# Kernel optimization log

Hardware: AMD Instinct MI355X
Metric: run time of the kernel (lower is better)

The kernel has to match this reference:

```python
import jax, jax.numpy as jnp
import numpy as np
from jax import lax

B, H, W, C = 2, 256, 256, 180
WS, SH, NH = 8, 4, 6
HD = C // NH          # 30
N = WS * WS           # 64
NW = (H // WS) * (W // WS)
HID = 4 * C
SCALE = HD ** -0.5
EPS = 1e-5


def _rel_pos_index(ws):
    coords = np.stack(np.meshgrid(np.arange(ws), np.arange(ws), indexing='ij'))  # [2,ws,ws]
    cf = coords.reshape(2, -1)
    rel = (cf[:, :, None] - cf[:, None, :]).transpose(1, 2, 0)  # [N,N,2]
    rel[:, :, 0] += ws - 1
    rel[:, :, 1] += ws - 1
    rel[:, :, 0] *= 2 * ws - 1
    return rel.sum(-1)  # [N,N]


def _attn_mask(h, w, ws, sh):
    img = np.zeros((h, w))
    sl = (slice(0, -ws), slice(-ws, -sh), slice(-sh, None))
    cnt = 0
    for hs in sl:
        for wsl in sl:
            img[hs, wsl] = cnt
            cnt += 1
    mw = img.reshape(h // ws, ws, w // ws, ws).transpose(0, 2, 1, 3).reshape(-1, ws * ws)  # [nW,N]
    d = mw[:, None, :] - mw[:, :, None]  # [nW,N,N]
    return np.where(d != 0, -100.0, 0.0).astype(np.float32)


REL_IDX = jnp.asarray(_rel_pos_index(WS))          # [N,N] int
MASK = jnp.asarray(_attn_mask(H, W, WS, SH))       # [nW,N,N] float


def _ln(x, g, b):
    m = jnp.mean(x, -1, keepdims=True)
    v = jnp.mean((x - m) ** 2, -1, keepdims=True)
    return (x - m) * lax.rsqrt(v + EPS) * g + b


def _win_part(x):  # (B,H,W,C) -> (B*nW,N,C)
    x = x.reshape(B, H // WS, WS, W // WS, WS, C).transpose(0, 1, 3, 2, 4, 5)
    return x.reshape(-1, N, C)


def _win_rev(w):  # (B*nW,N,C) -> (B,H,W,C)
    x = w.reshape(B, H // WS, W // WS, WS, WS, C).transpose(0, 1, 3, 2, 4, 5)
    return x.reshape(B, H, W, C)


def setup_inputs() -> dict:
    key = jax.random.key(0)
    ks = jax.random.split(key, 8)
    s = 0.02
    return {
        'x': jax.random.normal(ks[0], (B, H * W, C), jnp.float32),
        'norm1_g': jnp.ones((C,), jnp.float32),
        'norm1_b': jnp.zeros((C,), jnp.float32),
        'qkv_w': jax.random.normal(ks[1], (C, 3 * C), jnp.float32) * s,
        'qkv_b': jnp.zeros((3 * C,), jnp.float32),
        'rel_pos_table': jax.random.normal(ks[2], ((2 * WS - 1) ** 2, NH), jnp.float32) * s,
        'proj_w': jax.random.normal(ks[3], (C, C), jnp.float32) * s,
        'proj_b': jnp.zeros((C,), jnp.float32),
        'norm2_g': jnp.ones((C,), jnp.float32),
        'norm2_b': jnp.zeros((C,), jnp.float32),
        'fc1_w': jax.random.normal(ks[4], (C, HID), jnp.float32) * s,
        'fc1_b': jnp.zeros((HID,), jnp.float32),
        'dw_w': jax.random.normal(ks[5], (HID, 1, 3, 3), jnp.float32) * s,
        'dw_b': jnp.zeros((HID,), jnp.float32),
        'fc2_w': jax.random.normal(ks[6], (HID, C), jnp.float32) * s,
        'fc2_b': jnp.zeros((C,), jnp.float32),
    }


def reference(x, norm1_g, norm1_b, qkv_w, qkv_b, rel_pos_table, proj_w, proj_b,
              norm2_g, norm2_b, fc1_w, fc1_b, dw_w, dw_b, fc2_w, fc2_b):
    shortcut = x
    h = _ln(x, norm1_g, norm1_b).reshape(B, H, W, C)
    h = jnp.roll(h, (-SH, -SH), axis=(1, 2))           # cyclic shift
    xw = _win_part(h)                                   # [B*nW, N, C]

    qkv = (xw @ qkv_w + qkv_b).reshape(-1, N, 3, NH, HD).transpose(2, 0, 3, 1, 4)
    q, k, v = qkv[0] * SCALE, qkv[1], qkv[2]            # [B_,NH,N,HD]
    attn = jnp.einsum('bhnd,bhmd->bhnm', q, k)          # [B_,NH,N,N]

    bias = rel_pos_table[REL_IDX.reshape(-1)].reshape(N, N, NH).transpose(2, 0, 1)
    attn = attn + bias[None]
    attn = attn.reshape(B, NW, NH, N, N) + MASK[None, :, None]
    attn = jax.nn.softmax(attn.reshape(-1, NH, N, N), axis=-1)

    out = jnp.einsum('bhnm,bhmd->bhnd', attn, v).transpose(0, 2, 1, 3).reshape(-1, N, C)
    out = out @ proj_w + proj_b
    out = jnp.roll(_win_rev(out), (SH, SH), axis=(1, 2)).reshape(B, H * W, C)
    x = shortcut + out

    # MLP with depthwise-conv interleave
    m = _ln(x, norm2_g, norm2_b)
    m = jax.nn.gelu(m @ fc1_w + fc1_b, approximate=False)   # [B,L,HID]
    mc = m.transpose(0, 2, 1).reshape(B, HID, H, W)
    mc = lax.conv_general_dilated(mc, dw_w, (1, 1), 'SAME',
                                  feature_group_count=HID,
                                  dimension_numbers=('NCHW', 'OIHW', 'NCHW'))
    mc = mc + dw_b[None, :, None, None]
    m = jax.nn.gelu(mc.reshape(B, HID, H * W).transpose(0, 2, 1), approximate=False)
    m = m @ fc2_w + fc2_b
    return x + m
```

## Files before the change

### kernel.cpp

```cpp
#include <hip/hip_runtime.h>
#include <hip/hip_bf16.h>


using short8 = __attribute__((ext_vector_type(8))) short;
using f32x4  = __attribute__((ext_vector_type(4))) float;

constexpr int   ROWS   = 131072;
constexpr float SCALE_ = 0.18257418583505536f;

constexpr size_t OFF_WQ    = 0;
constexpr size_t OFF_WP    = OFF_WQ   + 576*192*2;
constexpr size_t OFF_WF1   = OFF_WP   + 192*192*2;
constexpr size_t OFF_WF2T  = OFF_WF1  + 768*192*2;
constexpr size_t OFF_BQ    = OFF_WF2T + 192*768*2;
constexpr size_t OFF_BP    = OFF_BQ   + 576*4;
constexpr size_t OFF_BF1   = OFF_BP   + 192*4;
constexpr size_t OFF_BF2   = OFF_BF1  + 768*4;
constexpr size_t OFF_BIASF = OFF_BF2  + 192*4;
constexpr size_t OFF_WDWT  = OFF_BIASF + 6*4096*4;
constexpr size_t OFF_BDW   = OFF_WDWT + 9*768*4;
constexpr size_t OFF_R1    = 1048576;
constexpr size_t SZ_R      = (size_t)ROWS * 192 * 2;
constexpr size_t OFF_R2    = OFF_R1 + SZ_R;
constexpr size_t OFF_R3    = OFF_R2 + SZ_R;
constexpr size_t WS_NEEDED = OFF_R3 + SZ_R;
static_assert(OFF_BDW + 768*4 <= OFF_R1, "weights overlap R1");
static_assert((size_t)66*256*768*2 <= SZ_R, "m1 band overflows R2");

__device__ __forceinline__ unsigned short f2bf(float f) {
    __hip_bfloat16 h = __float2bfloat16(f);
    return *reinterpret_cast<unsigned short*>(&h);
}
__device__ __forceinline__ float bf2f(unsigned short u) {
    union { unsigned int i; float f; } x; x.i = ((unsigned int)u) << 16; return x.f;
}
__device__ __forceinline__ float gelu_f(float x) {
    return 0.5f * x * (1.0f + erff(x * 0.70710678118654752f));
}

__global__ __launch_bounds__(256) void prep_kernel(
    const float* __restrict__ qkv_w, const float* __restrict__ qkv_b,
    const float* __restrict__ proj_w, const float* __restrict__ proj_b,
    const float* __restrict__ fc1_w, const float* __restrict__ fc1_b,
    const float* __restrict__ fc2_w, const float* __restrict__ fc2_b,
    const float* __restrict__ rpt,
    const float* __restrict__ dw_w, const float* __restrict__ dw_b,
    unsigned short* __restrict__ wq, unsigned short* __restrict__ wp,
    unsigned short* __restrict__ wf1, unsigned short* __restrict__ wf2t,
    float* __restrict__ bq, float* __restrict__ bp,
    float* __restrict__ bf1, float* __restrict__ bf2,
    float* __restrict__ biasf,
    float* __restrict__ wdwT, float* __restrict__ bdw)
{
    int idx = blockIdx.x * 256 + threadIdx.x;
    constexpr int E1 = 576*192;
    constexpr int E2 = E1 + 192*192;
    constexpr int E3 = E2 + 768*192;
    constexpr int E4 = E3 + 192*768;
    constexpr int E5 = E4 + 576;
    constexpr int E6 = E5 + 192;
    constexpr int E7 = E6 + 768;
    constexpr int E8 = E7 + 192;
    constexpr int E9 = E8 + 6*4096;
    constexpr int E10 = E9 + 9*768;
    constexpr int E11 = E10 + 768;
    if (idx < E1) {
        int n = idx / 192, kx = idx % 192;
        float v = 0.f;
        if (n < 540 && kx < 180) { v = qkv_w[kx*540 + n]; if (n < 180) v *= SCALE_; }
        wq[idx] = f2bf(v);
    } else if (idx < E2) {
        int j = idx - E1; int n = j / 192, kx = j % 192;
        wp[j] = f2bf((n < 180 && kx < 180) ? proj_w[kx*180 + n] : 0.f);
    } else if (idx < E3) {
        int j = idx - E2; int n = j / 192, kx = j % 192;
        wf1[j] = f2bf((n < 720 && kx < 180) ? fc1_w[kx*720 + n] : 0.f);
    } else if (idx < E4) {
        int j = idx - E3; int n = j / 768, kx = j % 768;
        wf2t[j] = f2bf((n < 180 && kx < 720) ? fc2_w[kx*180 + n] : 0.f);
    } else if (idx < E5) {
        int n = idx - E4;
        float v = (n < 540) ? qkv_b[n] : 0.f; if (n < 180) v *= SCALE_;
        bq[n] = v;
    } else if (idx < E6) {
        int n = idx - E5; bp[n] = (n < 180) ? proj_b[n] : 0.f;
    } else if (idx < E7) {
        int n = idx - E6; bf1[n] = (n < 720) ? fc1_b[n] : 0.f;
    } else if (idx < E8) {
        int n = idx - E7; bf2[n] = (n < 180) ? fc2_b[n] : 0.f;
    } else if (idx < E9) {
        int j = idx - E8;
        int hh = j / 4096, t = j & 4095;
        int n = t >> 6, m = t & 63;
        int rid = ((n>>3) - (m>>3) + 7)*15 + ((n&7) - (m&7) + 7);
        biasf[j] = rpt[rid*6 + hh];
    } else if (idx < E10) {
        int j = idx - E9;
        int tap = j / 768, c = j % 768;
        wdwT[j] = (c < 720) ? dw_w[c*9 + tap] : 0.f;
    } else if (idx < E11) {
        int c = idx - E10;
        bdw[c] = (c < 720) ? dw_b[c] : 0.f;
    }
}

template<int ROLL>
__global__ __launch_bounds__(256) void ln_kernel(const float* __restrict__ x,
    const float* __restrict__ g, const float* __restrict__ bsh,
    unsigned short* __restrict__ out)
{
    int row  = blockIdx.x * 4 + (threadIdx.x >> 6);
    int lane = threadIdx.x & 63;
    size_t src;
    if (ROLL) {
        int b    = row >> 16;
        int widx = (row >> 6) & 1023;
        int n    = row & 63;
        int hr   = ((widx >> 5) << 3) + (n >> 3);
        int wr   = ((widx & 31) << 3) + (n & 7);
        int h2   = (hr + 4) & 255;
        int w2   = (wr + 4) & 255;
        src = ((size_t)b << 16) + (h2 << 8) + w2;
    } else {
        src = (size_t)row;
    }
    const float* xr = x + src * 180;
    float v1 = xr[lane];
    float v2 = xr[lane + 64];
    float v3 = (lane < 52) ? xr[lane + 128] : 0.0f;
    float s1 = v1 + v2 + v3;
    float s2 = v1*v1 + v2*v2 + v3*v3;
    #pragma unroll
    for (int o = 32; o > 0; o >>= 1) { s1 += __shfl_xor(s1, o); s2 += __shfl_xor(s2, o); }
    float mean = s1 * (1.0f/180.0f);
    float var  = s2 * (1.0f/180.0f) - mean*mean;
    float rstd = rsqrtf(var + 1e-5f);
    unsigned short* orow = out + (size_t)row * 192;
    orow[lane]      = f2bf((v1 - mean)*rstd*g[lane]      + bsh[lane]);
    orow[lane + 64] = f2bf((v2 - mean)*rstd*g[lane + 64] + bsh[lane + 64]);
    if (lane < 52) orow[lane + 128] = f2bf((v3 - mean)*rstd*g[lane + 128] + bsh[lane + 128]);
    else           orow[lane + 128] = 0;
}

__global__ __launch_bounds__(256) void zeropad_kernel(unsigned int* q, unsigned int* k, unsigned int* v)
{
    int idx = blockIdx.x * 256 + threadIdx.x;
    int wid = idx / 192, t = idx % 192;
    if (t < 64)       q[wid*1024 + t*16 + 15] = 0;
    else if (t < 128) k[wid*1024 + (t-64)*16 + 15] = 0;
    else              v[wid*1024 + 960 + (t-128)] = 0;
}

template<int MODE>
__global__ __launch_bounds__(256) void gemm64(
    const unsigned short* __restrict__ A, const unsigned short* __restrict__ Bt,
    const float* __restrict__ bias, int K, int lda, int ldb, int ldo,
    unsigned short* __restrict__ oq, unsigned short* __restrict__ ok2,
    unsigned short* __restrict__ ov, unsigned short* __restrict__ obf)
{
    __shared__ __align__(16) unsigned short As[64*40];
    __shared__ __align__(16) unsigned short Bs[64*40];
    const int tid  = threadIdx.x;
    const int bn   = blockIdx.x, bm = blockIdx.y;
    const int lane = tid & 63;
    const int wv   = tid >> 6;
    const int wr   = wv >> 1, wc = wv & 1;
    const int l15  = lane & 15, l4 = lane >> 4;
    const int r    = tid >> 2;
    const int kk   = (tid & 3) << 3;

    f32x4 acc[2][2];
    #pragma unroll
    for (int i = 0; i < 2; i++)
        #pragma unroll
        for (int j = 0; j < 2; j++) acc[i][j] = f32x4{0.f, 0.f, 0.f, 0.f};

    const size_t abase = (size_t)(bm*64 + r) * (size_t)lda + kk;
    const size_t bbase = (size_t)(bn*64 + r) * (size_t)ldb + kk;
    const int lds_wi = r*40 + kk;

    for (int kt = 0; kt < K; kt += 32) {
        *(uint4*)&As[lds_wi] = *(const uint4*)&A[abase + kt];
        *(uint4*)&Bs[lds_wi] = *(const uint4*)&Bt[bbase + kt];
        __syncthreads();
        short8 af[2], bf[2];
        #pragma unroll
        for (int fm = 0; fm < 2; fm++) af[fm] = *(const short8*)&As[(wr*32 + fm*16 + l15)*40 + l4*8];
        #pragma unroll
        for (int fn = 0; fn < 2; fn++) bf[fn] = *(const short8*)&Bs[(wc*32 + fn*16 + l15)*40 + l4*8];
        #pragma unroll
        for (int fm = 0; fm < 2; fm++)
            #pragma unroll
            for (int fn = 0; fn < 2; fn++)
                acc[fm][fn] = __builtin_amdgcn_mfma_f32_16x16x32_bf16(af[fm], bf[fn], acc[fm][fn], 0, 0, 0);
        __syncthreads();
    }

    #pragma unroll
    for (int fm = 0; fm < 2; fm++) {
      #pragma unroll
      for (int fn = 0; fn < 2; fn++) {
        #pragma unroll
        for (int rr = 0; rr < 4; rr++) {
            int grow  = bm*64 + wr*32 + fm*16 + l4*4 + rr;
            int gcol  = bn*64 + wc*32 + fn*16 + l15;
            float v = acc[fm][fn][rr] + bias[gcol];
            if (MODE == 0) {
                if (gcol < 540) {
                    int which = (gcol >= 360) ? 2 : (gcol >= 180 ? 1 : 0);
                    int cc = gcol - which*180;
                    int hh = cc / 30;
                    int dd = cc - hh*30;
                    size_t wid = (size_t)(grow >> 6)*6 + hh;
                    if (which == 0)      oq [wid*2048 + (grow & 63)*32 + dd] = f2bf(v);
                    else if (which == 1) ok2[wid*2048 + (grow & 63)*32 + dd] = f2bf(v);
                    else                 ov [wid*2048 + dd*64 + (grow & 63)] = f2bf(v);
                }
            } else {
                obf[(size_t)grow*ldo + gcol] = f2bf(gelu_f(v));
            }
        }
      }
    }
}

template<int M_BLK, int MODE>
__global__ __launch_bounds__(256) void gemmN192(
    const unsigned short* __restrict__ A, const unsigned short* __restrict__ Bt,
    const float* __restrict__ bias, int K, int lda, int ldb,
    const float* __restrict__ xres, float* __restrict__ out)
{
    constexpr int MB = M_BLK / 16;
    constexpr int LDS_STAGE = (M_BLK*40 + 192*40) * 2;
    constexpr int LDS_CST   = M_BLK * 180 * 4;
    constexpr int LDSZ = LDS_STAGE > LDS_CST ? LDS_STAGE : LDS_CST;
    __shared__ __align__(16) char lds[LDSZ];
    unsigned short* As = (unsigned short*)lds;
    unsigned short* Bs = As + M_BLK*40;
    float* Cst = (float*)lds;

    const int tid  = threadIdx.x;
    const int bm   = blockIdx.x;
    const int lane = tid & 63;
    const int wv   = tid >> 6;
    const int l15  = lane & 15, l4 = lane >> 4;
    const int r    = tid >> 2;
    const int kk   = (tid & 3) << 3;

    f32x4 acc[MB][3];
    #pragma unroll
    for (int m = 0; m < MB; m++)
        #pragma unroll
        for (int nb = 0; nb < 3; nb++) acc[m][nb] = f32x4{0.f,0.f,0.f,0.f};

    const size_t abase = (size_t)(bm*M_BLK + r) * (size_t)lda + kk;
    const size_t bbase = (size_t)r * (size_t)ldb + kk;

    for (int kt = 0; kt < K; kt += 32) {
        if (M_BLK == 64 || tid < M_BLK*4)
            *(uint4*)&As[r*40 + kk] = *(const uint4*)&A[abase + kt];
        #pragma unroll
        for (int jj = 0; jj < 3; jj++)
            *(uint4*)&Bs[(r + jj*64)*40 + kk] = *(const uint4*)&Bt[bbase + (size_t)jj*64*ldb + kt];
        __syncthreads();
        short8 af[MB], bf[3];
        #pragma unroll
        for (int m = 0; m < MB; m++) af[m] = *(const short8*)&As[(m*16 + l15)*40 + l4*8];
        #pragma unroll
        for (int nb = 0; nb < 3; nb++) bf[nb] = *(const short8*)&Bs[(wv*48 + nb*16 + l15)*40 + l4*8];
        #pragma unroll
        for (int m = 0; m < MB; m++)
            #pragma unroll
            for (int nb = 0; nb < 3; nb++)
                acc[m][nb] = __builtin_amdgcn_mfma_f32_16x16x32_bf16(af[m], bf[nb], acc[m][nb], 0, 0, 0);
        __syncthreads();
    }

    #pragma unroll
    for (int m = 0; m < MB; m++)
      #pragma unroll
      for (int nb = 0; nb < 3; nb++)
        #pragma unroll
        for (int rr = 0; rr < 4; rr++) {
            int tok = m*16 + l4*4 + rr;
            int col = wv*48 + nb*16 + l15;
            if (col < 180) Cst[tok*180 + col] = acc[m][nb][rr];
        }
    __syncthreads();

    for (int idx = tid; idx < M_BLK*4; idx += 256) {
        int tok = idx >> 2, j = idx & 3;
        int c0  = j * 48;
        int cnt = (j == 3) ? 36 : 48;
        size_t orow;
        if (MODE == 0) {
            int grow = bm*M_BLK + tok;
            int wig  = grow >> 6;
            int b_   = wig >> 10, wi = wig & 1023, ti = grow & 63;
            int h2   = (((wi >> 5) << 3) + (ti >> 3) + 4) & 255;
            int w2   = (((wi & 31) << 3) + (ti & 7) + 4) & 255;
            orow = ((size_t)b_ << 16) + (h2 << 8) + w2;
        } else {
            orow = (size_t)(bm*M_BLK + tok);
        }
        float*       op = out  + orow*180 + c0;
        const float* cp = &Cst[tok*180 + c0];
        const float* bb = bias + c0;
        if (MODE == 0) {
            const float* xp = xres + orow*180 + c0;
            for (int i = 0; i < cnt; i += 4) {
                f32x4 ov = *(const f32x4*)&xp[i] + *(const f32x4*)&cp[i] + *(const f32x4*)&bb[i];
                *(f32x4*)&op[i] = ov;
            }
        } else {
            for (int i = 0; i < cnt; i += 4) {
                f32x4 ov = *(const f32x4*)&op[i];
                ov += *(const f32x4*)&cp[i] + *(const f32x4*)&bb[i];
                *(f32x4*)&op[i] = ov;
            }
        }
    }
}

__global__ __launch_bounds__(64) void attn_kernel(
    const unsigned short* __restrict__ q, const unsigned short* __restrict__ k,
    const unsigned short* __restrict__ vt, const float* __restrict__ biasf,
    unsigned short* __restrict__ aout)
{
    __shared__ __align__(16) unsigned short P[64*72];
    const int wid  = blockIdx.x;
    const int b_   = wid / 6, hh = wid % 6;
    const int lane = threadIdx.x;
    const int l15  = lane & 15, l4 = lane >> 4;

    const unsigned short* qb = q  + (size_t)wid*2048;
    const unsigned short* kb = k  + (size_t)wid*2048;
    const unsigned short* vb = vt + (size_t)wid*2048;

    short8 qf[4], kf[4];
    #pragma unroll
    for (int t = 0; t < 4; t++) {
        qf[t] = *(const short8*)&qb[(t*16 + l15)*32 + l4*8];
        kf[t] = *(const short8*)&kb[(t*16 + l15)*32 + l4*8];
    }
    f32x4 s[4][4];
    #pragma unroll
    for (int m = 0; m < 4; m++)
        #pragma unroll
        for (int n = 0; n < 4; n++)
            s[m][n] = __builtin_amdgcn_mfma_f32_16x16x32_bf16(qf[m], kf[n], f32x4{0.f,0.f,0.f,0.f}, 0, 0, 0);

    const int wi = b_ & 1023;
    const int wh = wi >> 5, ww = wi & 31;
    const bool edge = (wh == 31) || (ww == 31);
    const float* bh = biasf + hh*4096;
    #pragma unroll
    for (int m = 0; m < 4; m++) {
      #pragma unroll
      for (int rr = 0; rr < 4; rr++) {
        int ni = m*16 + l4*4 + rr;
        int ln_n = 0;
        if (edge) {
            int rh = (wh < 31) ? 0 : (((ni >> 3) < 4) ? 1 : 2);
            int rw = (ww < 31) ? 0 : (((ni & 7) < 4) ? 1 : 2);
            ln_n = rh*3 + rw;
        }
        #pragma unroll
        for (int n = 0; n < 4; n++) {
            int mj = n*16 + l15;
            float add = bh[ni*64 + mj];
            if (edge) {
                int rh = (wh < 31) ? 0 : (((mj >> 3) < 4) ? 1 : 2);
                int rw = (ww < 31) ? 0 : (((mj & 7) < 4) ? 1 : 2);
                if (rh*3 + rw != ln_n) add -= 100.0f;
            }
            s[m][n][rr] += add;
        }
      }
    }
    #pragma unroll
    for (int m = 0; m < 4; m++) {
      #pragma unroll
      for (int rr = 0; rr < 4; rr++) {
        float mx = fmaxf(fmaxf(s[m][0][rr], s[m][1][rr]), fmaxf(s[m][2][rr], s[m][3][rr]));
        #pragma unroll
        for (int o = 8; o > 0; o >>= 1) mx = fmaxf(mx, __shfl_xor(mx, o));
        float sum = 0.f;
        #pragma unroll
        for (int n = 0; n < 4; n++) { float e = __expf(s[m][n][rr] - mx); s[m][n][rr] = e; sum += e; }
        #pragma unroll
        for (int o = 8; o > 0; o >>= 1) sum += __shfl_xor(sum, o);
        float inv = 1.0f / sum;
        int ni = m*16 + l4*4 + rr;
        #pragma unroll
        for (int n = 0; n < 4; n++) P[ni*72 + n*16 + l15] = f2bf(s[m][n][rr] * inv);
      }
    }
    __syncthreads();
    f32x4 po[4][2];
    #pragma unroll
    for (int m = 0; m < 4; m++)
        #pragma unroll
        for (int n = 0; n < 2; n++) po[m][n] = f32x4{0.f,0.f,0.f,0.f};
    #pragma unroll
    for (int ks = 0; ks < 2; ks++) {
        short8 pf[4], vf[2];
        #pragma unroll
        for (int m = 0; m < 4; m++) pf[m] = *(const short8*)&P[(m*16 + l15)*72 + ks*32 + l4*8];
        #pragma unroll
        for (int n = 0; n < 2; n++) vf[n] = *(const short8*)&vb[(n*16 + l15)*64 + ks*32 + l4*8];
        #pragma unroll
        for (int m = 0; m < 4; m++)
            #pragma unroll
            for (int n = 0; n < 2; n++)
                po[m][n] = __builtin_amdgcn_mfma_f32_16x16x32_bf16(pf[m], vf[n], po[m][n], 0, 0, 0);
    }
    #pragma unroll
    for (int m = 0; m < 4; m++)
      #pragma unroll
      for (int n = 0; n < 2; n++)
        #pragma unroll
        for (int rr = 0; rr < 4; rr++) {
            int ni = m*16 + l4*4 + rr;
            int dd = n*16 + l15;
            if (dd < 30)
                aout[((size_t)b_*64 + ni)*192 + hh*30 + dd] = f2bf(po[m][n][rr]);
        }
}

__global__ __launch_bounds__(256) void dwconv_band(
    const unsigned short* __restrict__ m1, const float* __restrict__ wT,
    const float* __restrict__ bias, int h0, unsigned short* __restrict__ m2)
{
    const int hl  = blockIdx.x;
    const int t   = threadIdx.x;
    const int cg  = t & 31;
    const int pl  = t >> 5;
    const int w0  = blockIdx.y * 64 + pl * 8;
    const int c   = blockIdx.z * 256 + cg * 8;

    float acc[8][8];
    float bv[8];
    *(f32x4*)&bv[0] = *(const f32x4*)&bias[c];
    *(f32x4*)&bv[4] = *(const f32x4*)&bias[c + 4];
    #pragma unroll
    for (int p = 0; p < 8; p++)
        #pragma unroll
        for (int i = 0; i < 8; i++) acc[p][i] = bv[i];

    const short8 zv = {0,0,0,0,0,0,0,0};
    #pragma unroll
    for (int dh = -1; dh <= 1; dh++) {
        int hg = h0 + hl + dh;
        if (hg < 0 || hg > 255) continue;
        const unsigned short* rb = m1 + (size_t)(hl + 1 + dh) * 256 * 768 + c;
        float f[10][8];
        #pragma unroll
        for (int j = 0; j < 10; j++) {
            int w2 = w0 - 1 + j;
            short8 v = (w2 < 0 || w2 > 255) ? zv : *(const short8*)&rb[(size_t)w2*768];
            #pragma unroll
            for (int i = 0; i < 8; i++) f[j][i] = bf2f((unsigned short)v[i]);
        }
        #pragma unroll
        for (int dw2 = 0; dw2 < 3; dw2++) {
            const float* wrow = wT + ((dh+1)*3 + dw2)*768 + c;
            float wt[8];
            *(f32x4*)&wt[0] = *(const f32x4*)&wrow[0];
            *(f32x4*)&wt[4] = *(const f32x4*)&wrow[4];
            #pragma unroll
            for (int p = 0; p < 8; p++)
                #pragma unroll
                for (int i = 0; i < 8; i++)
                    acc[p][i] += f[p + dw2][i] * wt[i];
        }
    }
    unsigned short* ob = m2 + ((size_t)hl*256 + w0)*768 + c;
    #pragma unroll
    for (int p = 0; p < 8; p++) {
        short8 o;
        #pragma unroll
        for (int i = 0; i < 8; i++) o[i] = (short)f2bf(gelu_f(acc[p][i]));
        *(short8*)&ob[(size_t)p*768] = o;
    }
}

extern "C" void kernel_launch(void* const* d_in, const int* in_sizes, int n_in,
                              void* d_out, int out_size, void* d_ws, size_t ws_size,
                              hipStream_t stream) {
    (void)in_sizes; (void)n_in; (void)out_size;
    if (ws_size < WS_NEEDED) return;
    const float* x      = (const float*)d_in[0];
    const float* n1g    = (const float*)d_in[1];
    const float* n1b    = (const float*)d_in[2];
    const float* qkv_w  = (const float*)d_in[3];
    const float* qkv_b  = (const float*)d_in[4];
    const float* rpt    = (const float*)d_in[5];
    const float* proj_w = (const float*)d_in[6];
    const float* proj_b = (const float*)d_in[7];
    const float* n2g    = (const float*)d_in[8];
    const float* n2b    = (const float*)d_in[9];
    const float* fc1_w  = (const float*)d_in[10];
    const float* fc1_b  = (const float*)d_in[11];
    const float* dw_w   = (const float*)d_in[12];
    const float* dw_b   = (const float*)d_in[13];
    const float* fc2_w  = (const float*)d_in[14];
    const float* fc2_b  = (const float*)d_in[15];
    float* out = (float*)d_out;
    char*  ws  = (char*)d_ws;

    unsigned short* wq   = (unsigned short*)(ws + OFF_WQ);
    unsigned short* wp   = (unsigned short*)(ws + OFF_WP);
    unsigned short* wf1  = (unsigned short*)(ws + OFF_WF1);
    unsigned short* wf2t = (unsigned short*)(ws + OFF_WF2T);
    float* bq    = (float*)(ws + OFF_BQ);
    float* bp    = (float*)(ws + OFF_BP);
    float* bf1   = (float*)(ws + OFF_BF1);
    float* bf2   = (float*)(ws + OFF_BF2);
    float* biasf = (float*)(ws + OFF_BIASF);
    float* wdwT  = (float*)(ws + OFF_WDWT);
    float* bdw   = (float*)(ws + OFF_BDW);
    unsigned short* R1 = (unsigned short*)(ws + OFF_R1);
    unsigned short* R2 = (unsigned short*)(ws + OFF_R2);
    unsigned short* R3 = (unsigned short*)(ws + OFF_R3);
    unsigned short* qp = (unsigned short*)d_out;

    prep_kernel<<<1861, 256, 0, stream>>>(qkv_w, qkv_b, proj_w, proj_b, fc1_w, fc1_b,
                                          fc2_w, fc2_b, rpt, dw_w, dw_b,
                                          wq, wp, wf1, wf2t,
                                          bq, bp, bf1, bf2, biasf, wdwT, bdw);
    ln_kernel<1><<<32768, 256, 0, stream>>>(x, n1g, n1b, R1);
    gemm64<0><<<dim3(9, 2048), 256, 0, stream>>>(R1, wq, bq, 192, 192, 192, 0,
                                                 qp, R2, R3, nullptr);
    zeropad_kernel<<<9216, 256, 0, stream>>>((unsigned int*)qp, (unsigned int*)R2, (unsigned int*)R3);
    attn_kernel<<<12288, 64, 0, stream>>>(qp, R2, R3, biasf, R1);
    gemmN192<64, 0><<<2048, 256, 0, stream>>>(R1, wp, bp, 192, 192, 192, x, out);
    ln_kernel<0><<<32768, 256, 0, stream>>>(out, n2g, n2b, R1);
    for (int band = 0; band < 8; ++band) {
        const int b_img   = band >> 2;
        const int h0      = (band & 3) * 64;
        const int h_start = (h0 == 0) ? 0 : h0 - 1;
        const int h_end   = (h0 + 64 < 256) ? (h0 + 65) : 256;
        const int n_rows  = h_end - h_start;
        const int moff    = (h0 == 0) ? 1 : 0;
        const size_t arow0 = ((size_t)b_img*256 + h_start) * 256;
        const size_t pix0  = ((size_t)b_img*256 + h0) * 256;
        gemm64<2><<<dim3(12, n_rows*4), 256, 0, stream>>>(
            R1 + arow0*192, wf1, bf1, 192, 192, 192, 768,
            nullptr, nullptr, nullptr, R2 + (size_t)moff*256*768);
        dwconv_band<<<dim3(64, 4, 3), 256, 0, stream>>>(R2, wdwT, bdw, h0, R3);
        gemmN192<32, 1><<<512, 256, 0, stream>>>(
            R3, wf2t, bf2, 768, 768, 768, nullptr, out + pix0*180);
    }
}
```

Measured before the change: 936.6 us.

## Keep A tile resident in LDS and loop over all N blocks per workgroup

The QKV and fc1 GEMMs now launch one workgroup per 64-row M block. Each workgroup loads its whole 64x192 A tile into LDS once, then loops over every 64-column N block, staging the full K=192 B tile per iteration. This removes the repeated A reloads across the N grid dimension and cuts per-K-step barriers. The cost is a much smaller grid (fewer workgroups, less parallelism), larger LDS use (about 60KB), and serialized N iterations in each block.

After: 1.031 ms. 10.1% more time.

```diff
diff --git a/kernel.cpp b/kernel.cpp
--- a/kernel.cpp
+++ b/kernel.cpp
@@ -151,17 +151,17 @@
     else              v[wid*1024 + 960 + (t-128)] = 0;
 }
 
-template<int MODE>
-__global__ __launch_bounds__(256) void gemm64(
+template<int MODE, int NBN>
+__global__ __launch_bounds__(256) void gemm_bnloop(
     const unsigned short* __restrict__ A, const unsigned short* __restrict__ Bt,
-    const float* __restrict__ bias, int K, int lda, int ldb, int ldo,
+    const float* __restrict__ bias,
     unsigned short* __restrict__ oq, unsigned short* __restrict__ ok2,
     unsigned short* __restrict__ ov, unsigned short* __restrict__ obf)
 {
-    __shared__ __align__(16) unsigned short As[64*40];
-    __shared__ __align__(16) unsigned short Bs[64*40];
+    __shared__ __align__(16) unsigned short As[6*64*40];
+    __shared__ __align__(16) unsigned short Bs[6*64*40];
     const int tid  = threadIdx.x;
-    const int bn   = blockIdx.x, bm = blockIdx.y;
+    const int bm   = blockIdx.x;
     const int lane = tid & 63;
     const int wv   = tid >> 6;
     const int wr   = wv >> 1, wc = wv & 1;
@@ -169,58 +169,64 @@
     const int r    = tid >> 2;
     const int kk   = (tid & 3) << 3;
 
-    f32x4 acc[2][2];
-    #pragma unroll
-    for (int i = 0; i < 2; i++)
-        #pragma unroll
-        for (int j = 0; j < 2; j++) acc[i][j] = f32x4{0.f, 0.f, 0.f, 0.f};
-
-    const size_t abase = (size_t)(bm*64 + r) * (size_t)lda + kk;
-    const size_t bbase = (size_t)(bn*64 + r) * (size_t)ldb + kk;
-    const int lds_wi = r*40 + kk;
-
-    for (int kt = 0; kt < K; kt += 32) {
-        *(uint4*)&As[lds_wi] = *(const uint4*)&A[abase + kt];
-        *(uint4*)&Bs[lds_wi] = *(const uint4*)&Bt[bbase + kt];
+    const size_t abase = (size_t)(bm*64 + r) * 192 + kk;
+    #pragma unroll
+    for (int kt = 0; kt < 6; kt++)
+        *(uint4*)&As[kt*2560 + r*40 + kk] = *(const uint4*)&A[abase + kt*32];
+
+    const size_t bstep = (size_t)r * 192 + kk;
+    for (int bn = 0; bn < NBN; bn++) {
+        #pragma unroll
+        for (int kt = 0; kt < 6; kt++)
+            *(uint4*)&Bs[kt*2560 + r*40 + kk] = *(const uint4*)&Bt[(size_t)bn*64*192 + bstep + kt*32];
         __syncthreads();
-        short8 af[2], bf[2];
-        #pragma unroll
-        for (int fm = 0; fm < 2; fm++) af[fm] = *(const short8*)&As[(wr*32 + fm*16 + l15)*40 + l4*8];
-        #pragma unroll
-        for (int fn = 0; fn < 2; fn++) bf[fn] = *(const short8*)&Bs[(wc*32 + fn*16 + l15)*40 + l4*8];
-        #pragma unroll
-        for (int fm = 0; fm < 2; fm++)
-            #pragma unroll
-            for (int fn = 0; fn < 2; fn++)
-                acc[fm][fn] = __builtin_amdgcn_mfma_f32_16x16x32_bf16(af[fm], bf[fn], acc[fm][fn], 0, 0, 0);
+
+        f32x4 acc[2][2];
+        #pragma unroll
+        for (int i = 0; i < 2; i++)
+            #pragma unroll
+            for (int j = 0; j < 2; j++) acc[i][j] = f32x4{0.f,0.f,0.f,0.f};
+        #pragma unroll
+        for (int kt = 0; kt < 6; kt++) {
+            short8 af[2], bf[2];
+            #pragma unroll
+            for (int fm = 0; fm < 2; fm++) af[fm] = *(const short8*)&As[kt*2560 + (wr*32 + fm*16 + l15)*40 + l4*8];
+            #pragma unroll
+            for (int fn = 0; fn < 2; fn++) bf[fn] = *(const short8*)&Bs[kt*2560 + (wc*32 + fn*16 + l15)*40 + l4*8];
+            #pragma unroll
+            for (int fm = 0; fm < 2; fm++)
+                #pragma unroll
+                for (int fn = 0; fn < 2; fn++)
+                    acc[fm][fn] = __builtin_amdgcn_mfma_f32_16x16x32_bf16(af[fm], bf[fn], acc[fm][fn], 0, 0, 0);
+        }
         __syncthreads();
-    }
-
-    #pragma unroll
-    for (int fm = 0; fm < 2; fm++) {
-      #pragma unroll
-      for (int fn = 0; fn < 2; fn++) {
-        #pragma unroll
-        for (int rr = 0; rr < 4; rr++) {
-            int grow  = bm*64 + wr*32 + fm*16 + l4*4 + rr;
-            int gcol  = bn*64 + wc*32 + fn*16 + l15;
-            float v = acc[fm][fn][rr] + bias[gcol];
-            if (MODE == 0) {
-                if (gcol < 540) {
-                    int which = (gcol >= 360) ? 2 : (gcol >= 180 ? 1 : 0);
-                    int cc = gcol - which*180;
-                    int hh = cc / 30;
-                    int dd = cc - hh*30;
-                    size_t wid = (size_t)(grow >> 6)*6 + hh;
-                    if (which == 0)      oq [wid*2048 + (grow & 63)*32 + dd] = f2bf(v);
-                    else if (which == 1) ok2[wid*2048 + (grow & 63)*32 + dd] = f2bf(v);
-                    else                 ov [wid*2048 + dd*64 + (grow & 63)] = f2bf(v);
+
+        #pragma unroll
+        for (int fm = 0; fm < 2; fm++) {
+          #pragma unroll
+          for (int fn = 0; fn < 2; fn++) {
+            #pragma unroll
+            for (int rr = 0; rr < 4; rr++) {
+                int grow = bm*64 + wr*32 + fm*16 + l4*4 + rr;
+                int gcol = bn*64 + wc*32 + fn*16 + l15;
+                float v = acc[fm][fn][rr] + bias[gcol];
+                if (MODE == 0) {
+                    if (gcol < 540) {
+                        int which = (gcol >= 360) ? 2 : (gcol >= 180 ? 1 : 0);
+                        int cc = gcol - which*180;
+                        int hh = cc / 30;
+                        int dd = cc - hh*30;
+                        size_t wid = (size_t)(grow >> 6)*6 + hh;
+                        if (which == 0)      oq [wid*2048 + (grow & 63)*32 + dd] = f2bf(v);
+                        else if (which == 1) ok2[wid*2048 + (grow & 63)*32 + dd] = f2bf(v);
+                        else                 ov [wid*2048 + dd*64 + (grow & 63)] = f2bf(v);
+                    }
+                } else {
+                    obf[(size_t)grow*768 + gcol] = f2bf(gelu_f(v));
                 }
-            } else {
-                obf[(size_t)grow*ldo + gcol] = f2bf(gelu_f(v));
             }
-        }
-      }
+          }
+        }
     }
 }
 
@@ -530,8 +536,7 @@
                                           wq, wp, wf1, wf2t,
                                           bq, bp, bf1, bf2, biasf, wdwT, bdw);
     ln_kernel<1><<<32768, 256, 0, stream>>>(x, n1g, n1b, R1);
-    gemm64<0><<<dim3(9, 2048), 256, 0, stream>>>(R1, wq, bq, 192, 192, 192, 0,
-                                                 qp, R2, R3, nullptr);
+    gemm_bnloop<0, 9><<<2048, 256, 0, stream>>>(R1, wq, bq, qp, R2, R3, nullptr);
     zeropad_kernel<<<9216, 256, 0, stream>>>((unsigned int*)qp, (unsigned int*)R2, (unsigned int*)R3);
     attn_kernel<<<12288, 64, 0, stream>>>(qp, R2, R3, biasf, R1);
     gemmN192<64, 0><<<2048, 256, 0, stream>>>(R1, wp, bp, 192, 192, 192, x, out);
@@ -545,8 +550,8 @@
         const int moff    = (h0 == 0) ? 1 : 0;
         const size_t arow0 = ((size_t)b_img*256 + h_start) * 256;
         const size_t pix0  = ((size_t)b_img*256 + h0) * 256;
-        gemm64<2><<<dim3(12, n_rows*4), 256, 0, stream>>>(
-            R1 + arow0*192, wf1, bf1, 192, 192, 192, 768,
+        gemm_bnloop<2, 12><<<n_rows*4, 256, 0, stream>>>(
+            R1 + arow0*192, wf1, bf1,
             nullptr, nullptr, nullptr, R2 + (size_t)moff*256*768);
         dwconv_band<<<dim3(64, 4, 3), 256, 0, stream>>>(R2, wdwT, bdw, h0, R3);
         gemmN192<32, 1><<<512, 256, 0, stream>>>(
```

## Fuse QKV projection with window attention in one per-window kernel

Applied to the files above, without the earlier changes.

Replaces the separate QKV GEMM, zero-pad kernel and per-head attention kernel with one kernel per window (6 waves, one per head). It computes Q/K/V directly into LDS using a head-interleaved, padded weight layout, then runs QK^T, bias/mask, softmax and PV in place, writing the output over the input rows. This removes the global round trip of Q/K/V and two launches. In exchange it uses large LDS (~78KB) and many registers, which limits occupancy. Weight B-fragments are read straight from global memory. The fc1 GEMM is also specialized and its grid order swapped so M blocks vary fastest.

Result: faster. 822.2 us, median of 3 (-12.2%).

```diff
diff --git a/kernel.cpp b/kernel.cpp
--- a/kernel.cpp
+++ b/kernel.cpp
@@ -45,9 +45,9 @@
     const float* __restrict__ fc2_w, const float* __restrict__ fc2_b,
     const float* __restrict__ rpt,
     const float* __restrict__ dw_w, const float* __restrict__ dw_b,
-    unsigned short* __restrict__ wq, unsigned short* __restrict__ wp,
+    unsigned short* __restrict__ wq2, unsigned short* __restrict__ wp,
     unsigned short* __restrict__ wf1, unsigned short* __restrict__ wf2t,
-    float* __restrict__ bq, float* __restrict__ bp,
+    float* __restrict__ bq2, float* __restrict__ bp,
     float* __restrict__ bf1, float* __restrict__ bf2,
     float* __restrict__ biasf,
     float* __restrict__ wdwT, float* __restrict__ bdw)
@@ -66,9 +66,14 @@
     constexpr int E11 = E10 + 768;
     if (idx < E1) {
         int n = idx / 192, kx = idx % 192;
+        int hh = n / 96, rem = n % 96;
+        int w  = rem / 32, c = rem % 32;
         float v = 0.f;
-        if (n < 540 && kx < 180) { v = qkv_w[kx*540 + n]; if (n < 180) v *= SCALE_; }
-        wq[idx] = f2bf(v);
+        if (c < 30 && kx < 180) {
+            v = qkv_w[kx*540 + w*180 + hh*30 + c];
+            if (w == 0) v *= SCALE_;
+        }
+        wq2[idx] = f2bf(v);
     } else if (idx < E2) {
         int j = idx - E1; int n = j / 192, kx = j % 192;
         wp[j] = f2bf((n < 180 && kx < 180) ? proj_w[kx*180 + n] : 0.f);
@@ -80,8 +85,11 @@
         wf2t[j] = f2bf((n < 180 && kx < 720) ? fc2_w[kx*180 + n] : 0.f);
     } else if (idx < E5) {
         int n = idx - E4;
-        float v = (n < 540) ? qkv_b[n] : 0.f; if (n < 180) v *= SCALE_;
-        bq[n] = v;
+        int hh = n / 96, rem = n % 96;
+        int w  = rem / 32, c = rem % 32;
+        float v = 0.f;
+        if (c < 30) { v = qkv_b[w*180 + hh*30 + c]; if (w == 0) v *= SCALE_; }
+        bq2[n] = v;
     } else if (idx < E6) {
         int n = idx - E5; bp[n] = (n < 180) ? proj_b[n] : 0.f;
     } else if (idx < E7) {
@@ -142,26 +150,234 @@
     else           orow[lane + 128] = 0;
 }
 
-__global__ __launch_bounds__(256) void zeropad_kernel(unsigned int* q, unsigned int* k, unsigned int* v)
+__global__ __launch_bounds__(384, 3) void fused_qkv_attn(
+    unsigned short* __restrict__ xw,
+    const unsigned short* __restrict__ wq2, const float* __restrict__ bq2,
+    const float* __restrict__ biasf)
 {
-    int idx = blockIdx.x * 256 + threadIdx.x;
-    int wid = idx / 192, t = idx % 192;
-    if (t < 64)       q[wid*1024 + t*16 + 15] = 0;
-    else if (t < 128) k[wid*1024 + (t-64)*16 + 15] = 0;
-    else              v[wid*1024 + 960 + (t-128)] = 0;
-}
-
-template<int MODE>
-__global__ __launch_bounds__(256) void gemm64(
+    __shared__ __align__(16) unsigned short lds[39936];
+    unsigned short* AsQ = lds;
+    unsigned short* KS  = lds + 15360;
+    unsigned short* VT  = lds + 27648;
+    unsigned short* P   = lds;
+
+    const int bm   = blockIdx.x;
+    const int tid  = threadIdx.x;
+    const int hh   = tid >> 6;
+    const int lane = tid & 63;
+    const int l15  = lane & 15, l4 = lane >> 4;
+
+    {
+        const unsigned short* Arow = xw + (size_t)bm * 12288;
+        #pragma unroll
+        for (int j = 0; j < 4; j++) {
+            int c   = tid + j*384;
+            int row = c / 24;
+            int s   = (c % 24) * 8;
+            int kt  = s >> 5, kk = s & 31;
+            *(uint4*)&AsQ[kt*2560 + row*40 + kk] = *(const uint4*)&Arow[row*192 + s];
+        }
+    }
+    __syncthreads();
+
+    f32x4 qa[2][4];
+    #pragma unroll
+    for (int ct = 0; ct < 2; ct++)
+        #pragma unroll
+        for (int m = 0; m < 4; m++) qa[ct][m] = f32x4{0.f,0.f,0.f,0.f};
+    {
+        #pragma unroll
+        for (int kt = 0; kt < 6; kt++) {
+            short8 af[4];
+            #pragma unroll
+            for (int m = 0; m < 4; m++) af[m] = *(const short8*)&AsQ[kt*2560 + (m*16 + l15)*40 + l4*8];
+            #pragma unroll
+            for (int ct = 0; ct < 2; ct++) {
+                short8 bf = *(const short8*)&wq2[(size_t)(hh*96 + ct*16 + l15)*192 + kt*32 + l4*8];
+                #pragma unroll
+                for (int m = 0; m < 4; m++)
+                    qa[ct][m] = __builtin_amdgcn_mfma_f32_16x16x32_bf16(af[m], bf, qa[ct][m], 0, 0, 0);
+            }
+        }
+    }
+    {
+        f32x4 ka[2][4];
+        #pragma unroll
+        for (int ct = 0; ct < 2; ct++)
+            #pragma unroll
+            for (int m = 0; m < 4; m++) ka[ct][m] = f32x4{0.f,0.f,0.f,0.f};
+        #pragma unroll
+        for (int kt = 0; kt < 6; kt++) {
+            short8 af[4];
+            #pragma unroll
+            for (int m = 0; m < 4; m++) af[m] = *(const short8*)&AsQ[kt*2560 + (m*16 + l15)*40 + l4*8];
+            #pragma unroll
+            for (int ct = 0; ct < 2; ct++) {
+                short8 bf = *(const short8*)&wq2[(size_t)(hh*96 + 32 + ct*16 + l15)*192 + kt*32 + l4*8];
+                #pragma unroll
+                for (int m = 0; m < 4; m++)
+                    ka[ct][m] = __builtin_amdgcn_mfma_f32_16x16x32_bf16(af[m], bf, ka[ct][m], 0, 0, 0);
+            }
+        }
+        #pragma unroll
+        for (int ct = 0; ct < 2; ct++)
+          #pragma unroll
+          for (int m = 0; m < 4; m++)
+            #pragma unroll
+            for (int rr = 0; rr < 4; rr++) {
+                int tok = m*16 + l4*4 + rr;
+                int dd  = ct*16 + l15;
+                KS[hh*2048 + tok*32 + dd] = f2bf(ka[ct][m][rr] + bq2[hh*96 + 32 + dd]);
+            }
+    }
+    {
+        f32x4 va[2][4];
+        #pragma unroll
+        for (int ct = 0; ct < 2; ct++)
+            #pragma unroll
+            for (int m = 0; m < 4; m++) va[ct][m] = f32x4{0.f,0.f,0.f,0.f};
+        #pragma unroll
+        for (int kt = 0; kt < 6; kt++) {
+            short8 af[4];
+            #pragma unroll
+            for (int m = 0; m < 4; m++) af[m] = *(const short8*)&AsQ[kt*2560 + (m*16 + l15)*40 + l4*8];
+            #pragma unroll
+            for (int ct = 0; ct < 2; ct++) {
+                short8 bf = *(const short8*)&wq2[(size_t)(hh*96 + 64 + ct*16 + l15)*192 + kt*32 + l4*8];
+                #pragma unroll
+                for (int m = 0; m < 4; m++)
+                    va[ct][m] = __builtin_amdgcn_mfma_f32_16x16x32_bf16(af[m], bf, va[ct][m], 0, 0, 0);
+            }
+        }
+        #pragma unroll
+        for (int ct = 0; ct < 2; ct++)
+          #pragma unroll
+          for (int m = 0; m < 4; m++)
+            #pragma unroll
+            for (int rr = 0; rr < 4; rr++) {
+                int tok = m*16 + l4*4 + rr;
+                int dd  = ct*16 + l15;
+                int tsw = tok ^ ((dd & 7) << 3);
+                VT[hh*2048 + dd*64 + tsw] = f2bf(va[ct][m][rr] + bq2[hh*96 + 64 + dd]);
+            }
+    }
+    __syncthreads();
+
+    #pragma unroll
+    for (int ct = 0; ct < 2; ct++)
+      #pragma unroll
+      for (int m = 0; m < 4; m++)
+        #pragma unroll
+        for (int rr = 0; rr < 4; rr++) {
+            int tok = m*16 + l4*4 + rr;
+            int dd  = ct*16 + l15;
+            AsQ[hh*2048 + tok*32 + dd] = f2bf(qa[ct][m][rr] + bq2[hh*96 + dd]);
+        }
+
+    short8 qf[4], kf[4];
+    #pragma unroll
+    for (int t = 0; t < 4; t++) {
+        qf[t] = *(const short8*)&AsQ[hh*2048 + (t*16 + l15)*32 + l4*8];
+        kf[t] = *(const short8*)&KS [hh*2048 + (t*16 + l15)*32 + l4*8];
+    }
+    __syncthreads();
+
+    f32x4 s[4][4];
+    #pragma unroll
+    for (int m = 0; m < 4; m++)
+        #pragma unroll
+        for (int n = 0; n < 4; n++)
+            s[m][n] = __builtin_amdgcn_mfma_f32_16x16x32_bf16(qf[m], kf[n], f32x4{0.f,0.f,0.f,0.f}, 0, 0, 0);
+
+    const int wi = bm & 1023;
+    const int wh = wi >> 5, ww = wi & 31;
+    const bool edge = (wh == 31) || (ww == 31);
+    const float* bh = biasf + hh*4096;
+    #pragma unroll
+    for (int m = 0; m < 4; m++) {
+      #pragma unroll
+      for (int rr = 0; rr < 4; rr++) {
+        int ni = m*16 + l4*4 + rr;
+        int ln_n = 0;
+        if (edge) {
+            int rh = (wh < 31) ? 0 : (((ni >> 3) < 4) ? 1 : 2);
+            int rw = (ww < 31) ? 0 : (((ni & 7) < 4) ? 1 : 2);
+            ln_n = rh*3 + rw;
+        }
+        #pragma unroll
+        for (int n = 0; n < 4; n++) {
+            int mj = n*16 + l15;
+            float add = bh[ni*64 + mj];
+            if (edge) {
+                int rh = (wh < 31) ? 0 : (((mj >> 3) < 4) ? 1 : 2);
+                int rw = (ww < 31) ? 0 : (((mj & 7) < 4) ? 1 : 2);
+                if (rh*3 + rw != ln_n) add -= 100.0f;
+            }
+            s[m][n][rr] += add;
+        }
+      }
+    }
+    #pragma unroll
+    for (int m = 0; m < 4; m++) {
+      #pragma unroll
+      for (int rr = 0; rr < 4; rr++) {
+        float mx = fmaxf(fmaxf(s[m][0][rr], s[m][1][rr]), fmaxf(s[m][2][rr], s[m][3][rr]));
+        #pragma unroll
+        for (int o = 8; o > 0; o >>= 1) mx = fmaxf(mx, __shfl_xor(mx, o));
+        float sum = 0.f;
+        #pragma unroll
+        for (int n = 0; n < 4; n++) { float e = __expf(s[m][n][rr] - mx); s[m][n][rr] = e; sum += e; }
+        #pragma unroll
+        for (int o = 8; o > 0; o >>= 1) sum += __shfl_xor(sum, o);
+        float inv = 1.0f / sum;
+        int ni = m*16 + l4*4 + rr;
+        #pragma unroll
+        for (int n = 0; n < 4; n++) P[hh*4608 + ni*72 + n*16 + l15] = f2bf(s[m][n][rr] * inv);
+      }
+    }
+    f32x4 po[4][2];
+    #pragma unroll
+    for (int m = 0; m < 4; m++)
+        #pragma unroll
+        for (int n = 0; n < 2; n++) po[m][n] = f32x4{0.f,0.f,0.f,0.f};
+    #pragma unroll
+    for (int ksx = 0; ksx < 2; ksx++) {
+        short8 pf[4], vf[2];
+        #pragma unroll
+        for (int m = 0; m < 4; m++) pf[m] = *(const short8*)&P[hh*4608 + (m*16 + l15)*72 + ksx*32 + l4*8];
+        #pragma unroll
+        for (int n = 0; n < 2; n++) {
+            int dd  = n*16 + l15;
+            int g   = (ksx*4 + l4) ^ (dd & 7);
+            vf[n] = *(const short8*)&VT[hh*2048 + dd*64 + g*8];
+        }
+        #pragma unroll
+        for (int m = 0; m < 4; m++)
+            #pragma unroll
+            for (int n = 0; n < 2; n++)
+                po[m][n] = __builtin_amdgcn_mfma_f32_16x16x32_bf16(pf[m], vf[n], po[m][n], 0, 0, 0);
+    }
+    unsigned short* ob = xw + (size_t)bm * 12288;
+    #pragma unroll
+    for (int m = 0; m < 4; m++)
+      #pragma unroll
+      for (int n = 0; n < 2; n++)
+        #pragma unroll
+        for (int rr = 0; rr < 4; rr++) {
+            int ni = m*16 + l4*4 + rr;
+            int dd = n*16 + l15;
+            if (dd < 30) ob[ni*192 + hh*30 + dd] = f2bf(po[m][n][rr]);
+        }
+}
+
+__global__ __launch_bounds__(256) void fc1_gemm64(
     const unsigned short* __restrict__ A, const unsigned short* __restrict__ Bt,
-    const float* __restrict__ bias, int K, int lda, int ldb, int ldo,
-    unsigned short* __restrict__ oq, unsigned short* __restrict__ ok2,
-    unsigned short* __restrict__ ov, unsigned short* __restrict__ obf)
+    const float* __restrict__ bias, unsigned short* __restrict__ obf)
 {
     __shared__ __align__(16) unsigned short As[64*40];
     __shared__ __align__(16) unsigned short Bs[64*40];
     const int tid  = threadIdx.x;
-    const int bn   = blockIdx.x, bm = blockIdx.y;
+    const int bm   = blockIdx.x, bn = blockIdx.y;
     const int lane = tid & 63;
     const int wv   = tid >> 6;
     const int wr   = wv >> 1, wc = wv & 1;
@@ -175,11 +391,11 @@
         #pragma unroll
         for (int j = 0; j < 2; j++) acc[i][j] = f32x4{0.f, 0.f, 0.f, 0.f};
 
-    const size_t abase = (size_t)(bm*64 + r) * (size_t)lda + kk;
-    const size_t bbase = (size_t)(bn*64 + r) * (size_t)ldb + kk;
+    const size_t abase = (size_t)(bm*64 + r) * 192 + kk;
+    const size_t bbase = (size_t)(bn*64 + r) * 192 + kk;
     const int lds_wi = r*40 + kk;
 
-    for (int kt = 0; kt < K; kt += 32) {
+    for (int kt = 0; kt < 192; kt += 32) {
         *(uint4*)&As[lds_wi] = *(const uint4*)&A[abase + kt];
         *(uint4*)&Bs[lds_wi] = *(const uint4*)&Bt[bbase + kt];
         __syncthreads();
@@ -195,33 +411,16 @@
                 acc[fm][fn] = __builtin_amdgcn_mfma_f32_16x16x32_bf16(af[fm], bf[fn], acc[fm][fn], 0, 0, 0);
         __syncthreads();
     }
-
-    #pragma unroll
-    for (int fm = 0; fm < 2; fm++) {
+    #pragma unroll
+    for (int fm = 0; fm < 2; fm++)
       #pragma unroll
-      for (int fn = 0; fn < 2; fn++) {
+      for (int fn = 0; fn < 2; fn++)
         #pragma unroll
         for (int rr = 0; rr < 4; rr++) {
-            int grow  = bm*64 + wr*32 + fm*16 + l4*4 + rr;
-            int gcol  = bn*64 + wc*32 + fn*16 + l15;
-            float v = acc[fm][fn][rr] + bias[gcol];
-            if (MODE == 0) {
-                if (gcol < 540) {
-                    int which = (gcol >= 360) ? 2 : (gcol >= 180 ? 1 : 0);
-                    int cc = gcol - which*180;
-                    int hh = cc / 30;
-                    int dd = cc - hh*30;
-                    size_t wid = (size_t)(grow >> 6)*6 + hh;
-                    if (which == 0)      oq [wid*2048 + (grow & 63)*32 + dd] = f2bf(v);
-                    else if (which == 1) ok2[wid*2048 + (grow & 63)*32 + dd] = f2bf(v);
-                    else                 ov [wid*2048 + dd*64 + (grow & 63)] = f2bf(v);
-                }
-            } else {
-                obf[(size_t)grow*ldo + gcol] = f2bf(gelu_f(v));
-            }
-        }
-      }
-    }
+            int grow = bm*64 + wr*32 + fm*16 + l4*4 + rr;
+            int gcol = bn*64 + wc*32 + fn*16 + l15;
+            obf[(size_t)grow*768 + gcol] = f2bf(gelu_f(acc[fm][fn][rr] + bias[gcol]));
+        }
 }
 
 template<int M_BLK, int MODE>
@@ -320,112 +519,6 @@
             }
         }
     }
-}
-
-__global__ __launch_bounds__(64) void attn_kernel(
-    const unsigned short* __restrict__ q, const unsigned short* __restrict__ k,
-    const unsigned short* __restrict__ vt, const float* __restrict__ biasf,
-    unsigned short* __restrict__ aout)
-{
-    __shared__ __align__(16) unsigned short P[64*72];
-    const int wid  = blockIdx.x;
-    const int b_   = wid / 6, hh = wid % 6;
-    const int lane = threadIdx.x;
-    const int l15  = lane & 15, l4 = lane >> 4;
-
-    const unsigned short* qb = q  + (size_t)wid*2048;
-    const unsigned short* kb = k  + (size_t)wid*2048;
-    const unsigned short* vb = vt + (size_t)wid*2048;
-
-    short8 qf[4], kf[4];
-    #pragma unroll
-    for (int t = 0; t < 4; t++) {
-        qf[t] = *(const short8*)&qb[(t*16 + l15)*32 + l4*8];
-        kf[t] = *(const short8*)&kb[(t*16 + l15)*32 + l4*8];
-    }
-    f32x4 s[4][4];
-    #pragma unroll
-    for (int m = 0; m < 4; m++)
-        #pragma unroll
-        for (int n = 0; n < 4; n++)
-            s[m][n] = __builtin_amdgcn_mfma_f32_16x16x32_bf16(qf[m], kf[n], f32x4{0.f,0.f,0.f,0.f}, 0, 0, 0);
-
-    const int wi = b_ & 1023;
-    const int wh = wi >> 5, ww = wi & 31;
-    const bool edge = (wh == 31) || (ww == 31);
-    const float* bh = biasf + hh*4096;
-    #pragma unroll
-    for (int m = 0; m < 4; m++) {
-      #pragma unroll
-      for (int rr = 0; rr < 4; rr++) {
-        int ni = m*16 + l4*4 + rr;
-        int ln_n = 0;
-        if (edge) {
-            int rh = (wh < 31) ? 0 : (((ni >> 3) < 4) ? 1 : 2);
-            int rw = (ww < 31) ? 0 : (((ni & 7) < 4) ? 1 : 2);
-            ln_n = rh*3 + rw;
-        }
-        #pragma unroll
-        for (int n = 0; n < 4; n++) {
-            int mj = n*16 + l15;
-            float add = bh[ni*64 + mj];
-            if (edge) {
-                int rh = (wh < 31) ? 0 : (((mj >> 3) < 4) ? 1 : 2);
-                int rw = (ww < 31) ? 0 : (((mj & 7) < 4) ? 1 : 2);
-                if (rh*3 + rw != ln_n) add -= 100.0f;
-            }
-            s[m][n][rr] += add;
-        }
-      }
-    }
-    #pragma unroll
-    for (int m = 0; m < 4; m++) {
-      #pragma unroll
-      for (int rr = 0; rr < 4; rr++) {
-        float mx = fmaxf(fmaxf(s[m][0][rr], s[m][1][rr]), fmaxf(s[m][2][rr], s[m][3][rr]));
-        #pragma unroll
-        for (int o = 8; o > 0; o >>= 1) mx = fmaxf(mx, __shfl_xor(mx, o));
-        float sum = 0.f;
-        #pragma unroll
-        for (int n = 0; n < 4; n++) { float e = __expf(s[m][n][rr] - mx); s[m][n][rr] = e; sum += e; }
-        #pragma unroll
-        for (int o = 8; o > 0; o >>= 1) sum += __shfl_xor(sum, o);
-        float inv = 1.0f / sum;
-        int ni = m*16 + l4*4 + rr;
-        #pragma unroll
-        for (int n = 0; n < 4; n++) P[ni*72 + n*16 + l15] = f2bf(s[m][n][rr] * inv);
-      }
-    }
-    __syncthreads();
-    f32x4 po[4][2];
-    #pragma unroll
-    for (int m = 0; m < 4; m++)
-        #pragma unroll
-        for (int n = 0; n < 2; n++) po[m][n] = f32x4{0.f,0.f,0.f,0.f};
-    #pragma unroll
-    for (int ks = 0; ks < 2; ks++) {
-        short8 pf[4], vf[2];
-        #pragma unroll
-        for (int m = 0; m < 4; m++) pf[m] = *(const short8*)&P[(m*16 + l15)*72 + ks*32 + l4*8];
-        #pragma unroll
-        for (int n = 0; n < 2; n++) vf[n] = *(const short8*)&vb[(n*16 + l15)*64 + ks*32 + l4*8];
-        #pragma unroll
-        for (int m = 0; m < 4; m++)
-            #pragma unroll
-            for (int n = 0; n < 2; n++)
-                po[m][n] = __builtin_amdgcn_mfma_f32_16x16x32_bf16(pf[m], vf[n], po[m][n], 0, 0, 0);
-    }
-    #pragma unroll
-    for (int m = 0; m < 4; m++)
-      #pragma unroll
-      for (int n = 0; n < 2; n++)
-        #pragma unroll
-        for (int rr = 0; rr < 4; rr++) {
-            int ni = m*16 + l4*4 + rr;
-            int dd = n*16 + l15;
-            if (dd < 30)
-                aout[((size_t)b_*64 + ni)*192 + hh*30 + dd] = f2bf(po[m][n][rr]);
-        }
 }
 
 __global__ __launch_bounds__(256) void dwconv_band(
@@ -509,11 +602,11 @@
     float* out = (float*)d_out;
     char*  ws  = (char*)d_ws;
 
-    unsigned short* wq   = (unsigned short*)(ws + OFF_WQ);
+    unsigned short* wq2  = (unsigned short*)(ws + OFF_WQ);
     unsigned short* wp   = (unsigned short*)(ws + OFF_WP);
     unsigned short* wf1  = (unsigned short*)(ws + OFF_WF1);
     unsigned short* wf2t = (unsigned short*)(ws + OFF_WF2T);
-    float* bq    = (float*)(ws + OFF_BQ);
+    float* bq2   = (float*)(ws + OFF_BQ);
     float* bp    = (float*)(ws + OFF_BP);
     float* bf1   = (float*)(ws + OFF_BF1);
     float* bf2   = (float*)(ws + OFF_BF2);
@@ -523,17 +616,13 @@
     unsigned short* R1 = (unsigned short*)(ws + OFF_R1);
     unsigned short* R2 = (unsigned short*)(ws + OFF_R2);
     unsigned short* R3 = (unsigned short*)(ws + OFF_R3);
-    unsigned short* qp = (unsigned short*)d_out;
 
     prep_kernel<<<1861, 256, 0, stream>>>(qkv_w, qkv_b, proj_w, proj_b, fc1_w, fc1_b,
                                           fc2_w, fc2_b, rpt, dw_w, dw_b,
-                                          wq, wp, wf1, wf2t,
-                                          bq, bp, bf1, bf2, biasf, wdwT, bdw);
+                                          wq2, wp, wf1, wf2t,
+                                          bq2, bp, bf1, bf2, biasf, wdwT, bdw);
     ln_kernel<1><<<32768, 256, 0, stream>>>(x, n1g, n1b, R1);
-    gemm64<0><<<dim3(9, 2048), 256, 0, stream>>>(R1, wq, bq, 192, 192, 192, 0,
-                                                 qp, R2, R3, nullptr);
-    zeropad_kernel<<<9216, 256, 0, stream>>>((unsigned int*)qp, (unsigned int*)R2, (unsigned int*)R3);
-    attn_kernel<<<12288, 64, 0, stream>>>(qp, R2, R3, biasf, R1);
+    fused_qkv_attn<<<2048, 384, 0, stream>>>(R1, wq2, bq2, biasf);
     gemmN192<64, 0><<<2048, 256, 0, stream>>>(R1, wp, bp, 192, 192, 192, x, out);
     ln_kernel<0><<<32768, 256, 0, stream>>>(out, n2g, n2b, R1);
     for (int band = 0; band < 8; ++band) {
@@ -545,9 +634,8 @@
         const int moff    = (h0 == 0) ? 1 : 0;
         const size_t arow0 = ((size_t)b_img*256 + h_start) * 256;
         const size_t pix0  = ((size_t)b_img*256 + h0) * 256;
-        gemm64<2><<<dim3(12, n_rows*4), 256, 0, stream>>>(
-            R1 + arow0*192, wf1, bf1, 192, 192, 192, 768,
-            nullptr, nullptr, nullptr, R2 + (size_t)moff*256*768);
+        fc1_gemm64<<<dim3(n_rows*4, 12), 256, 0, stream>>>(
+            R1 + arow0*192, wf1, bf1, R2 + (size_t)moff*256*768);
         dwconv_band<<<dim3(64, 4, 3), 256, 0, stream>>>(R2, wdwT, bdw, h0, R3);
         gemmN192<32, 1><<<512, 256, 0, stream>>>(
             R3, wf2t, bf2, 768, 768, 768, nullptr, out + pix0*180);
```
